# Optimization experiments

Hardware: AMD Instinct MI355X
Metric: run time of the kernel (lower is better)

## Reference

```python
import jax, jax.numpy as jnp
import numpy as np
from jax import lax

D = 1024
K = 3
LN_EPS = 1e-5


def setup_inputs() -> dict:
    key = jax.random.key(0)
    ks = jax.random.split(key, 8)
    B, T = 8, 4096
    x = jax.random.normal(ks[0], (B, T, D), dtype=jnp.float32)
    s = 1.0 / np.sqrt(D)
    in_proj_w = jax.random.uniform(ks[1], (D, 2 * D), jnp.float32, -s, s)
    in_proj_b = jax.random.uniform(ks[2], (2 * D,), jnp.float32, -s, s)
    conv_w = jax.random.uniform(ks[3], (D, 1, K), jnp.float32, -1.0 / np.sqrt(K), 1.0 / np.sqrt(K))
    conv_b = jax.random.uniform(ks[4], (D,), jnp.float32, -1.0 / np.sqrt(K), 1.0 / np.sqrt(K))
    logit_a = jnp.zeros((D,), jnp.float32)
    ssm_b = jnp.full((D,), 0.1, jnp.float32)
    ssm_c = jnp.ones((D,), jnp.float32)
    ssm_d = jnp.zeros((D,), jnp.float32)
    out_proj_w = jax.random.uniform(ks[5], (D, D), jnp.float32, -s, s)
    out_proj_b = jax.random.uniform(ks[6], (D,), jnp.float32, -s, s)
    ln_w = jnp.ones((D,), jnp.float32)
    ln_b = jnp.zeros((D,), jnp.float32)
    return {"x": x, "in_proj_w": in_proj_w, "in_proj_b": in_proj_b,
            "conv_w": conv_w, "conv_b": conv_b, "logit_a": logit_a,
            "ssm_b": ssm_b, "ssm_c": ssm_c, "ssm_d": ssm_d,
            "out_proj_w": out_proj_w, "out_proj_b": out_proj_b,
            "ln_w": ln_w, "ln_b": ln_b}


def _dwconv(v, conv_w, conv_b):
    # v: (B, T, D) -> depthwise conv1d, kernel K, 'same' padding
    vt = jnp.transpose(v, (0, 2, 1))  # (B, D, T)
    out = lax.conv_general_dilated(
        vt, conv_w, window_strides=(1,), padding=[(K // 2, K // 2)],
        dimension_numbers=("NCH", "OIH", "NCH"), feature_group_count=D)
    out = out + conv_b[None, :, None]
    return jnp.transpose(out, (0, 2, 1))  # (B, T, D)


def reference(x, in_proj_w, in_proj_b, conv_w, conv_b, logit_a,
              ssm_b, ssm_c, ssm_d, out_proj_w, out_proj_b, ln_w, ln_b):
    B, T, _ = x.shape
    residual = x
    uv = x @ in_proj_w + in_proj_b                      # (B, T, 2D)
    u, v = uv[..., :D], uv[..., D:]
    v = jax.nn.silu(v)
    v_local = _dwconv(v, conv_w, conv_b)                # (B, T, D)

    a = jax.nn.sigmoid(logit_a).astype(v_local.dtype)
    # diagonal LTI scan: h_t = a*h_{t-1} + b*u_t ; y_t = c*h_t + d*u_t
    def step(h, vt):
        h = a * h + ssm_b * vt
        return h, ssm_c * h + ssm_d * vt
    h0 = jnp.zeros((B, D), v_local.dtype)
    _, y_seq = lax.scan(step, h0, jnp.transpose(v_local, (1, 0, 2)))
    y_seq = jnp.transpose(y_seq, (1, 0, 2))             # (B, T, D)

    out = u * jax.nn.silu(y_seq)
    out = out @ out_proj_w + out_proj_b                 # dropout: eval mode (identity)
    h = out + residual
    mu = jnp.mean(h, axis=-1, keepdims=True)
    var = jnp.mean(jnp.square(h - mu), axis=-1, keepdims=True)
    return (h - mu) * lax.rsqrt(var + LN_EPS) * ln_w + ln_b
```

## Files before the change

kernel.cpp:

```cpp
#include <hip/hip_runtime.h>
#include <cstdint>
#include <cstddef>

#define D_DIM   1024
#define TWO_D   2048
#define B_DIM   8
#define T_DIM   4096
#define BT_DIM  (B_DIM*T_DIM)
#define LN_EPS  1e-5f
#define NCHUNK  128
#define CLEN    (T_DIM/NCHUNK)

typedef __attribute__((ext_vector_type(8))) short bf16x8;
typedef __attribute__((ext_vector_type(4))) float f32x4;

__device__ __forceinline__ float bf2f(unsigned short u){
  union { unsigned int i; float f; } c; c.i = ((unsigned int)u) << 16; return c.f;
}
__device__ __forceinline__ unsigned short f2bf(float f){
  union { float f; unsigned int i; } c; c.f = f;
  unsigned int x = c.i;
  return (unsigned short)((x + 0x7fffu + ((x >> 16) & 1u)) >> 16);
}
__device__ __forceinline__ float sigmoidf_(float x){ return 1.f/(1.f+__expf(-x)); }
__device__ __forceinline__ float siluf_(float x){ return x/(1.f+__expf(-x)); }


__global__ void cvt_f32_bf16(const float* __restrict__ in, unsigned short* __restrict__ out, int n){
  int i = (blockIdx.x*blockDim.x + threadIdx.x)*4;
  const int stride = gridDim.x*blockDim.x*4;
  for (; i + 3 < n; i += stride){
    float4 f = *(const float4*)(in + i);
    ushort4 o; o.x=f2bf(f.x); o.y=f2bf(f.y); o.z=f2bf(f.z); o.w=f2bf(f.w);
    *(ushort4*)(out + i) = o;
  }
}

__global__ __launch_bounds__(256) void cvt_transpose(
    const float* __restrict__ W, unsigned short* __restrict__ Wt,
    int rows, int cols)
{
  __shared__ float tile[32][33];
  const int tx = threadIdx.x & 31;
  const int ty = threadIdx.x >> 5;
  const int tpc = cols >> 5;
  const int bc = blockIdx.x % tpc;
  const int br = blockIdx.x / tpc;
  const int gc = bc*32 + tx;
  const int gr = br*32;
#pragma unroll
  for (int i = 0; i < 32; i += 8)
    tile[ty + i][tx] = W[(size_t)(gr + ty + i)*cols + gc];
  __syncthreads();
#pragma unroll
  for (int i = 0; i < 32; i += 8)
    Wt[(size_t)(bc*32 + ty + i)*rows + gr + tx] = f2bf(tile[tx][ty + i]);
}

template<int EPI>
__global__ __launch_bounds__(512, 2) void gemm256(
    const unsigned short* __restrict__ A,
    const unsigned short* __restrict__ Bt,
    const float* __restrict__ bias,
    const float* __restrict__ resid,
    unsigned short* __restrict__ outU,
    unsigned short* __restrict__ outV,
    float* __restrict__ outF,
    const int K, const int nbn)
{
  __shared__ __align__(16) unsigned short sA[2][2][8192];
  __shared__ __align__(16) unsigned short sB[2][2][8192];

#define BARRIER()   __builtin_amdgcn_s_barrier()
#define FENCE()     __builtin_amdgcn_sched_barrier(0)
#define WAIT_VM4()  do { asm volatile("s_waitcnt vmcnt(4)"); FENCE(); } while(0)
#define WAIT_VM0()  do { asm volatile("s_waitcnt vmcnt(0)"); FENCE(); } while(0)

  const int tid  = threadIdx.x;
  const int lane = tid & 63;
  const int wv   = tid >> 6;
  const int wr   = wv >> 2;
  const int wc   = wv & 3;
  const int fr   = lane & 15;
  const int fq   = lane >> 4;

  const int nwg = gridDim.x;
  const int cpx = nwg >> 3;
  const int wg  = (blockIdx.x & 7) * cpx + (blockIdx.x >> 3);
  const int bm = wg / nbn, bn = wg % nbn;

  const unsigned short* Ag = A  + (size_t)bm * 256 * K;
  const unsigned short* Bg = Bt + (size_t)bn * 256 * K;

  const int r0  = tid >> 2;
  const int r1  = 128 + r0;
  const int c0  = tid & 3;
  const int cs0 = c0 ^ ((r0 >> 1) & 3);
  const int cs1 = c0 ^ ((r1 >> 1) & 3);
  const int ld0 = tid * 8;
  const int ld1 = (512 + tid) * 8;

#define STAGE(ARR, srcp, kofs)                                                           \
  do {                                                                                   \
    __builtin_amdgcn_global_load_lds(                                                    \
      (const __attribute__((address_space(1))) void*)((srcp) + (size_t)r0*K + (kofs) + cs0*8), \
      (__attribute__((address_space(3))) void*)(&(ARR)[ld0]), 16, 0, 0);                 \
    __builtin_amdgcn_global_load_lds(                                                    \
      (const __attribute__((address_space(1))) void*)((srcp) + (size_t)r1*K + (kofs) + cs1*8), \
      (__attribute__((address_space(3))) void*)(&(ARR)[ld1]), 16, 0, 0);                 \
  } while(0)

  const int swz  = fq ^ ((fr >> 1) & 3);
  const int offA = (wr*128 + fr) * 32 + swz * 8;
  const int offB = (wc*64  + fr) * 32 + swz * 8;

  f32x4 acc[8][4];
#pragma unroll
  for (int i = 0; i < 8; ++i)
#pragma unroll
    for (int j = 0; j < 4; ++j) acc[i][j] = {0.f,0.f,0.f,0.f};

  bf16x8 afr[8], bfr[4];

#define PHASE(PAR, KH, STAGE_STMT, TAIL_WAIT)                              \
  do {                                                                     \
    _Pragma("unroll")                                                      \
    for (int m2 = 0; m2 < 8; ++m2)                                         \
      afr[m2] = *(const bf16x8*)(&sA[PAR][KH][offA + m2*512]);             \
    _Pragma("unroll")                                                      \
    for (int n2 = 0; n2 < 4; ++n2)                                         \
      bfr[n2] = *(const bf16x8*)(&sB[PAR][KH][offB + n2*512]);             \
    STAGE_STMT;                                                            \
    BARRIER();                                                             \
    asm volatile("s_waitcnt lgkmcnt(0)");                                  \
    FENCE();                                                               \
    __builtin_amdgcn_s_setprio(1);                                         \
    _Pragma("unroll")                                                      \
    for (int m2 = 0; m2 < 8; ++m2)                                         \
      _Pragma("unroll")                                                    \
      for (int n2 = 0; n2 < 4; ++n2)                                       \
        acc[m2][n2] = __builtin_amdgcn_mfma_f32_16x16x32_bf16(             \
            afr[m2], bfr[n2], acc[m2][n2], 0, 0, 0);                       \
    __builtin_amdgcn_s_setprio(0);                                         \
    TAIL_WAIT;                                                             \
    BARRIER();                                                             \
  } while(0)

  const int npairs = K >> 7;

  STAGE(sA[0][0], Ag, 0);
  STAGE(sB[0][0], Bg, 0);
  STAGE(sA[0][1], Ag, 32);
  STAGE(sB[0][1], Bg, 32);
  WAIT_VM4();
  BARRIER();

  for (int i = 0; i < npairs - 1; ++i){
    const int kbO = ((i << 1) + 1) << 6;
    const int kbE = ((i << 1) + 2) << 6;
    PHASE(0, 0, { STAGE(sA[1][0], Ag, kbO);      STAGE(sB[1][0], Bg, kbO);      }, WAIT_VM4());
    PHASE(0, 1, { STAGE(sA[1][1], Ag, kbO + 32); STAGE(sB[1][1], Bg, kbO + 32); }, WAIT_VM4());
    PHASE(1, 0, { STAGE(sA[0][0], Ag, kbE);      STAGE(sB[0][0], Bg, kbE);      }, WAIT_VM4());
    PHASE(1, 1, { STAGE(sA[0][1], Ag, kbE + 32); STAGE(sB[0][1], Bg, kbE + 32); }, WAIT_VM4());
  }
  PHASE(0, 0, { STAGE(sA[1][0], Ag, K - 64); STAGE(sB[1][0], Bg, K - 64); }, WAIT_VM4());
  PHASE(0, 1, { STAGE(sA[1][1], Ag, K - 32); STAGE(sB[1][1], Bg, K - 32); }, WAIT_VM4());
  PHASE(1, 0, , WAIT_VM0());
  PHASE(1, 1, , );

  const int nb = bn*256 + wc*64;
  const int mb = bm*256 + wr*128;
  float bsv[4];
#pragma unroll
  for (int ni = 0; ni < 4; ++ni) bsv[ni] = bias[nb + ni*16 + fr];

  if (EPI == 0){
    const bool isV = (nb >= D_DIM);
    unsigned short* dst = isV ? (outV + (nb - D_DIM)) : (outU + nb);
#pragma unroll
    for (int mi = 0; mi < 8; ++mi){
#pragma unroll
      for (int j = 0; j < 4; ++j){
        const int m = mb + mi*16 + fq*4 + j;
        unsigned short* row = dst + (size_t)m*D_DIM + fr;
#pragma unroll
        for (int ni = 0; ni < 4; ++ni){
          float cv = acc[mi][ni][j] + bsv[ni];
          row[ni*16] = f2bf(isV ? siluf_(cv) : cv);
        }
      }
    }
  } else {
#pragma unroll
    for (int mi = 0; mi < 8; ++mi){
#pragma unroll
      for (int j = 0; j < 4; ++j){
        const int m = mb + mi*16 + fq*4 + j;
        const float* rrow = resid + (size_t)m*D_DIM + nb + fr;
        float* orow = outF + (size_t)m*D_DIM + nb + fr;
#pragma unroll
        for (int ni = 0; ni < 4; ++ni)
          orow[ni*16] = acc[mi][ni][j] + bsv[ni] + rrow[ni*16];
      }
    }
  }
#undef PHASE
#undef STAGE
#undef BARRIER
#undef FENCE
#undef WAIT_VM4
#undef WAIT_VM0
}

__global__ __launch_bounds__(256) void scan_a(
    const unsigned short* __restrict__ v,
    const float* __restrict__ conv_w, const float* __restrict__ conv_b,
    const float* __restrict__ logit_a, const float* __restrict__ ssm_b,
    float* __restrict__ hend)
{
  const int b = blockIdx.x / NCHUNK;
  const int c = blockIdx.x % NCHUNK;
  const int d0 = threadIdx.x * 4;
  const int t0 = c * CLEN;
  const unsigned short* vb = v + (size_t)b * T_DIM * D_DIM;

  float w0[4], w1[4], w2[4], av[4], bv[4], cb[4];
#pragma unroll
  for (int i=0;i<4;i++){
    w0[i] = conv_w[(d0+i)*3+0];
    w1[i] = conv_w[(d0+i)*3+1];
    w2[i] = conv_w[(d0+i)*3+2];
    cb[i] = conv_b[d0+i];
    av[i] = sigmoidf_(logit_a[d0+i]);
    bv[i] = ssm_b[d0+i];
  }
  float vm1[4], v0[4], h[4] = {0.f,0.f,0.f,0.f};
  if (t0 == 0){
#pragma unroll
    for (int i=0;i<4;i++) vm1[i]=0.f;
  } else {
    ushort4 u = *(const ushort4*)(vb + (size_t)(t0-1)*D_DIM + d0);
    vm1[0]=bf2f(u.x); vm1[1]=bf2f(u.y); vm1[2]=bf2f(u.z); vm1[3]=bf2f(u.w);
  }
  {
    ushort4 u = *(const ushort4*)(vb + (size_t)t0*D_DIM + d0);
    v0[0]=bf2f(u.x); v0[1]=bf2f(u.y); v0[2]=bf2f(u.z); v0[3]=bf2f(u.w);
  }
#pragma unroll 8
  for (int t = t0; t < t0 + CLEN; ++t){
    float vp1[4];
    if (t + 1 < T_DIM){
      ushort4 u = *(const ushort4*)(vb + (size_t)(t+1)*D_DIM + d0);
      vp1[0]=bf2f(u.x); vp1[1]=bf2f(u.y); vp1[2]=bf2f(u.z); vp1[3]=bf2f(u.w);
    } else { vp1[0]=vp1[1]=vp1[2]=vp1[3]=0.f; }
#pragma unroll
    for (int i=0;i<4;i++){
      float vl = w0[i]*vm1[i] + w1[i]*v0[i] + w2[i]*vp1[i] + cb[i];
      h[i] = av[i]*h[i] + bv[i]*vl;
      vm1[i]=v0[i]; v0[i]=vp1[i];
    }
  }
  float* he = hend + ((size_t)b*NCHUNK + c)*D_DIM + d0;
#pragma unroll
  for (int i=0;i<4;i++) he[i] = h[i];
}

__global__ void scan_fix(const float* __restrict__ hend, const float* __restrict__ logit_a,
                         float* __restrict__ hinit)
{
  int idx = blockIdx.x*blockDim.x + threadIdx.x;
  if (idx >= B_DIM*D_DIM) return;
  const int b = idx / D_DIM, d = idx % D_DIM;
  const float a  = sigmoidf_(logit_a[d]);
  const float aL = __powf(a, (float)CLEN);
  float h = 0.f;
  for (int c = 0; c < NCHUNK; ++c){
    hinit[((size_t)b*NCHUNK + c)*D_DIM + d] = h;
    h = aL*h + hend[((size_t)b*NCHUNK + c)*D_DIM + d];
  }
}

__global__ __launch_bounds__(256) void scan_c(
    const unsigned short* __restrict__ v,
    const unsigned short* __restrict__ ubuf,
    const float* __restrict__ conv_w, const float* __restrict__ conv_b,
    const float* __restrict__ logit_a, const float* __restrict__ ssm_b,
    const float* __restrict__ ssm_c, const float* __restrict__ ssm_d,
    const float* __restrict__ hinit,
    unsigned short* __restrict__ gated)
{
  const int b = blockIdx.x / NCHUNK;
  const int c = blockIdx.x % NCHUNK;
  const int d0 = threadIdx.x * 4;
  const int t0 = c * CLEN;
  const unsigned short* vb = v    + (size_t)b * T_DIM * D_DIM;
  const unsigned short* ub = ubuf + (size_t)b * T_DIM * D_DIM;
  unsigned short* gb       = gated+ (size_t)b * T_DIM * D_DIM;

  float w0[4], w1[4], w2[4], av[4], bv[4], cb[4], scv[4], sdv[4], h[4];
#pragma unroll
  for (int i=0;i<4;i++){
    w0[i] = conv_w[(d0+i)*3+0];
    w1[i] = conv_w[(d0+i)*3+1];
    w2[i] = conv_w[(d0+i)*3+2];
    cb[i] = conv_b[d0+i];
    av[i] = sigmoidf_(logit_a[d0+i]);
    bv[i] = ssm_b[d0+i];
    scv[i] = ssm_c[d0+i];
    sdv[i] = ssm_d[d0+i];
    h[i] = hinit[((size_t)b*NCHUNK + c)*D_DIM + d0 + i];
  }
  float vm1[4], v0[4];
  if (t0 == 0){
#pragma unroll
    for (int i=0;i<4;i++) vm1[i]=0.f;
  } else {
    ushort4 u = *(const ushort4*)(vb + (size_t)(t0-1)*D_DIM + d0);
    vm1[0]=bf2f(u.x); vm1[1]=bf2f(u.y); vm1[2]=bf2f(u.z); vm1[3]=bf2f(u.w);
  }
  {
    ushort4 u = *(const ushort4*)(vb + (size_t)t0*D_DIM + d0);
    v0[0]=bf2f(u.x); v0[1]=bf2f(u.y); v0[2]=bf2f(u.z); v0[3]=bf2f(u.w);
  }
#pragma unroll 8
  for (int t = t0; t < t0 + CLEN; ++t){
    float vp1[4];
    if (t + 1 < T_DIM){
      ushort4 u = *(const ushort4*)(vb + (size_t)(t+1)*D_DIM + d0);
      vp1[0]=bf2f(u.x); vp1[1]=bf2f(u.y); vp1[2]=bf2f(u.z); vp1[3]=bf2f(u.w);
    } else { vp1[0]=vp1[1]=vp1[2]=vp1[3]=0.f; }
    ushort4 uu = *(const ushort4*)(ub + (size_t)t*D_DIM + d0);
    float uf[4] = { bf2f(uu.x), bf2f(uu.y), bf2f(uu.z), bf2f(uu.w) };
    ushort4 go;
    unsigned short gtmp[4];
#pragma unroll
    for (int i=0;i<4;i++){
      float vl = w0[i]*vm1[i] + w1[i]*v0[i] + w2[i]*vp1[i] + cb[i];
      h[i] = av[i]*h[i] + bv[i]*vl;
      float y = scv[i]*h[i] + sdv[i]*vl;
      gtmp[i] = f2bf(uf[i] * siluf_(y));
      vm1[i]=v0[i]; v0[i]=vp1[i];
    }
    go.x=gtmp[0]; go.y=gtmp[1]; go.z=gtmp[2]; go.w=gtmp[3];
    *(ushort4*)(gb + (size_t)t*D_DIM + d0) = go;
  }
}

__global__ __launch_bounds__(256) void ln_kernel(
    float* __restrict__ io, const float* __restrict__ lw, const float* __restrict__ lb)
{
  __shared__ float rs[4], rq[4];
  const int row = blockIdx.x;
  const int tid = threadIdx.x;
  float* p = io + (size_t)row * D_DIM;
  float4 x = *(const float4*)(p + tid*4);
  float s = x.x + x.y + x.z + x.w;
  float q = x.x*x.x + x.y*x.y + x.z*x.z + x.w*x.w;
#pragma unroll
  for (int off = 32; off > 0; off >>= 1){
    s += __shfl_down(s, off, 64);
    q += __shfl_down(q, off, 64);
  }
  const int wv = tid >> 6;
  if ((tid & 63) == 0){ rs[wv] = s; rq[wv] = q; }
  __syncthreads();
  const float ts = rs[0]+rs[1]+rs[2]+rs[3];
  const float tq = rq[0]+rq[1]+rq[2]+rq[3];
  const float mu  = ts * (1.f/(float)D_DIM);
  const float var = tq * (1.f/(float)D_DIM) - mu*mu;
  const float inv = rsqrtf(var + LN_EPS);
  const float4 w4 = *(const float4*)(lw + tid*4);
  const float4 b4 = *(const float4*)(lb + tid*4);
  float4 o;
  o.x = (x.x-mu)*inv*w4.x + b4.x;
  o.y = (x.y-mu)*inv*w4.y + b4.y;
  o.z = (x.z-mu)*inv*w4.z + b4.z;
  o.w = (x.w-mu)*inv*w4.w + b4.w;
  *(float4*)(p + tid*4) = o;
}

extern "C" void kernel_launch(void* const* d_in, const int* in_sizes, int n_in,
                              void* d_out, int out_size, void* d_ws, size_t ws_size,
                              hipStream_t stream)
{
  const float* x     = (const float*)d_in[0];
  const float* w1    = (const float*)d_in[1];
  const float* b1    = (const float*)d_in[2];
  const float* convw = (const float*)d_in[3];
  const float* convb = (const float*)d_in[4];
  const float* la    = (const float*)d_in[5];
  const float* sb    = (const float*)d_in[6];
  const float* sc    = (const float*)d_in[7];
  const float* sd    = (const float*)d_in[8];
  const float* w2    = (const float*)d_in[9];
  const float* b2    = (const float*)d_in[10];
  const float* lw    = (const float*)d_in[11];
  const float* lb    = (const float*)d_in[12];
  float* out = (float*)d_out;

  char* ws = (char*)d_ws;
  unsigned short* xb    = (unsigned short*)(ws + 0);
  unsigned short* ubf   = (unsigned short*)(ws + 67108864);
  unsigned short* vbf   = (unsigned short*)(ws + 134217728);
  unsigned short* w1t   = (unsigned short*)(ws + 201326592);
  unsigned short* w2t   = (unsigned short*)(ws + 205520896);
  float*          hend  = (float*)(ws + 207618048);
  float*          hinit = (float*)(ws + 211812352);

  cvt_f32_bf16<<<2048, 256, 0, stream>>>(x, xb, BT_DIM*D_DIM);
  cvt_transpose<<<(D_DIM/32)*(TWO_D/32), 256, 0, stream>>>(w1, w1t, D_DIM, TWO_D);
  cvt_transpose<<<(D_DIM/32)*(D_DIM/32), 256, 0, stream>>>(w2, w2t, D_DIM, D_DIM);

  gemm256<0><<<dim3((BT_DIM/256)*(TWO_D/256)), 512, 0, stream>>>(
      xb, w1t, b1, nullptr, ubf, vbf, nullptr, D_DIM, TWO_D/256);

  scan_a<<<B_DIM*NCHUNK, 256, 0, stream>>>(vbf, convw, convb, la, sb, hend);
  scan_fix<<<(B_DIM*D_DIM + 255)/256, 256, 0, stream>>>(hend, la, hinit);
  scan_c<<<B_DIM*NCHUNK, 256, 0, stream>>>(vbf, ubf, convw, convb, la, sb, sc, sd, hinit, xb);

  gemm256<1><<<dim3((BT_DIM/256)*(D_DIM/256)), 512, 0, stream>>>(
      xb, w2t, b2, x, nullptr, nullptr, out, D_DIM, D_DIM/256);

  ln_kernel<<<BT_DIM, 256, 0, stream>>>(out, lw, lb);
}
```

Baseline: 426.9 us.

## Replace pipelined 256x256 GEMM with simple single-buffered 128x128 GEMM

The GEMM kernel moves from a 256x256 tile with 512 threads, double-buffered LDS and hand-scheduled phases (setprio, explicit waitcnt) to a 128x128 tile with 256 threads and a plain single-buffered load/sync/compute loop. The aim is higher occupancy and more workgroups. The cost is losing the overlap of global loads with MFMA and halving data reuse per tile, which raises global and LDS traffic. scan_fix also batches its 8 strided hend loads ahead of the serial recurrence to expose memory parallelism.

```diff
diff --git a/kernel.cpp b/kernel.cpp
--- a/kernel.cpp
+++ b/kernel.cpp
@@ -58,7 +58,7 @@
 }
 
 template<int EPI>
-__global__ __launch_bounds__(512, 2) void gemm256(
+__global__ __launch_bounds__(256, 4) void gemm128(
     const unsigned short* __restrict__ A,
     const unsigned short* __restrict__ Bt,
     const float* __restrict__ bias,
@@ -68,19 +68,14 @@
     float* __restrict__ outF,
     const int K, const int nbn)
 {
-  __shared__ __align__(16) unsigned short sA[2][2][8192];
-  __shared__ __align__(16) unsigned short sB[2][2][8192];
-
-#define BARRIER()   __builtin_amdgcn_s_barrier()
-#define FENCE()     __builtin_amdgcn_sched_barrier(0)
-#define WAIT_VM4()  do { asm volatile("s_waitcnt vmcnt(4)"); FENCE(); } while(0)
-#define WAIT_VM0()  do { asm volatile("s_waitcnt vmcnt(0)"); FENCE(); } while(0)
+  __shared__ __align__(16) unsigned short As[128*32];
+  __shared__ __align__(16) unsigned short Bs[128*32];
 
   const int tid  = threadIdx.x;
   const int lane = tid & 63;
   const int wv   = tid >> 6;
-  const int wr   = wv >> 2;
-  const int wc   = wv & 3;
+  const int wr   = wv >> 1;
+  const int wc   = wv & 1;
   const int fr   = lane & 15;
   const int fq   = lane >> 4;
 
@@ -89,16 +84,16 @@
   const int wg  = (blockIdx.x & 7) * cpx + (blockIdx.x >> 3);
   const int bm = wg / nbn, bn = wg % nbn;
 
-  const unsigned short* Ag = A  + (size_t)bm * 256 * K;
-  const unsigned short* Bg = Bt + (size_t)bn * 256 * K;
+  const unsigned short* Ag = A  + (size_t)bm * 128 * K;
+  const unsigned short* Bg = Bt + (size_t)bn * 128 * K;
 
   const int r0  = tid >> 2;
-  const int r1  = 128 + r0;
+  const int r1  = 64 + r0;
   const int c0  = tid & 3;
   const int cs0 = c0 ^ ((r0 >> 1) & 3);
   const int cs1 = c0 ^ ((r1 >> 1) & 3);
   const int ld0 = tid * 8;
-  const int ld1 = (512 + tid) * 8;
+  const int ld1 = (256 + tid) * 8;
 
 #define STAGE(ARR, srcp, kofs)                                                           \
   do {                                                                                   \
@@ -111,65 +106,36 @@
   } while(0)
 
   const int swz  = fq ^ ((fr >> 1) & 3);
-  const int offA = (wr*128 + fr) * 32 + swz * 8;
-  const int offB = (wc*64  + fr) * 32 + swz * 8;
-
-  f32x4 acc[8][4];
-#pragma unroll
-  for (int i = 0; i < 8; ++i)
+  const int offA = (wr*64 + fr) * 32 + swz * 8;
+  const int offB = (wc*64 + fr) * 32 + swz * 8;
+
+  f32x4 acc[4][4];
+#pragma unroll
+  for (int i = 0; i < 4; ++i)
 #pragma unroll
     for (int j = 0; j < 4; ++j) acc[i][j] = {0.f,0.f,0.f,0.f};
 
-  bf16x8 afr[8], bfr[4];
-
-#define PHASE(PAR, KH, STAGE_STMT, TAIL_WAIT)                              \
-  do {                                                                     \
-    _Pragma("unroll")                                                      \
-    for (int m2 = 0; m2 < 8; ++m2)                                         \
-      afr[m2] = *(const bf16x8*)(&sA[PAR][KH][offA + m2*512]);             \
-    _Pragma("unroll")                                                      \
-    for (int n2 = 0; n2 < 4; ++n2)                                         \
-      bfr[n2] = *(const bf16x8*)(&sB[PAR][KH][offB + n2*512]);             \
-    STAGE_STMT;                                                            \
-    BARRIER();                                                             \
-    asm volatile("s_waitcnt lgkmcnt(0)");                                  \
-    FENCE();                                                               \
-    __builtin_amdgcn_s_setprio(1);                                         \
-    _Pragma("unroll")                                                      \
-    for (int m2 = 0; m2 < 8; ++m2)                                         \
-      _Pragma("unroll")                                                    \
-      for (int n2 = 0; n2 < 4; ++n2)                                       \
-        acc[m2][n2] = __builtin_amdgcn_mfma_f32_16x16x32_bf16(             \
-            afr[m2], bfr[n2], acc[m2][n2], 0, 0, 0);                       \
-    __builtin_amdgcn_s_setprio(0);                                         \
-    TAIL_WAIT;                                                             \
-    BARRIER();                                                             \
-  } while(0)
-
-  const int npairs = K >> 7;
-
-  STAGE(sA[0][0], Ag, 0);
-  STAGE(sB[0][0], Bg, 0);
-  STAGE(sA[0][1], Ag, 32);
-  STAGE(sB[0][1], Bg, 32);
-  WAIT_VM4();
-  BARRIER();
-
-  for (int i = 0; i < npairs - 1; ++i){
-    const int kbO = ((i << 1) + 1) << 6;
-    const int kbE = ((i << 1) + 2) << 6;
-    PHASE(0, 0, { STAGE(sA[1][0], Ag, kbO);      STAGE(sB[1][0], Bg, kbO);      }, WAIT_VM4());
-    PHASE(0, 1, { STAGE(sA[1][1], Ag, kbO + 32); STAGE(sB[1][1], Bg, kbO + 32); }, WAIT_VM4());
-    PHASE(1, 0, { STAGE(sA[0][0], Ag, kbE);      STAGE(sB[0][0], Bg, kbE);      }, WAIT_VM4());
-    PHASE(1, 1, { STAGE(sA[0][1], Ag, kbE + 32); STAGE(sB[0][1], Bg, kbE + 32); }, WAIT_VM4());
-  }
-  PHASE(0, 0, { STAGE(sA[1][0], Ag, K - 64); STAGE(sB[1][0], Bg, K - 64); }, WAIT_VM4());
-  PHASE(0, 1, { STAGE(sA[1][1], Ag, K - 32); STAGE(sB[1][1], Bg, K - 32); }, WAIT_VM4());
-  PHASE(1, 0, , WAIT_VM0());
-  PHASE(1, 1, , );
-
-  const int nb = bn*256 + wc*64;
-  const int mb = bm*256 + wr*128;
+  for (int kt = 0; kt < K; kt += 32){
+    STAGE(As, Ag, kt);
+    STAGE(Bs, Bg, kt);
+    __syncthreads();
+
+    bf16x8 af[4], bf[4];
+#pragma unroll
+    for (int mi = 0; mi < 4; ++mi) af[mi] = *(const bf16x8*)(&As[offA + mi*512]);
+#pragma unroll
+    for (int ni = 0; ni < 4; ++ni) bf[ni] = *(const bf16x8*)(&Bs[offB + ni*512]);
+#pragma unroll
+    for (int mi = 0; mi < 4; ++mi)
+#pragma unroll
+      for (int ni = 0; ni < 4; ++ni)
+        acc[mi][ni] = __builtin_amdgcn_mfma_f32_16x16x32_bf16(af[mi], bf[ni], acc[mi][ni], 0, 0, 0);
+    __syncthreads();
+  }
+#undef STAGE
+
+  const int nb = bn*128 + wc*64;
+  const int mb = bm*128 + wr*64;
   float bsv[4];
 #pragma unroll
   for (int ni = 0; ni < 4; ++ni) bsv[ni] = bias[nb + ni*16 + fr];
@@ -178,7 +144,7 @@
     const bool isV = (nb >= D_DIM);
     unsigned short* dst = isV ? (outV + (nb - D_DIM)) : (outU + nb);
 #pragma unroll
-    for (int mi = 0; mi < 8; ++mi){
+    for (int mi = 0; mi < 4; ++mi){
 #pragma unroll
       for (int j = 0; j < 4; ++j){
         const int m = mb + mi*16 + fq*4 + j;
@@ -192,7 +158,7 @@
     }
   } else {
 #pragma unroll
-    for (int mi = 0; mi < 8; ++mi){
+    for (int mi = 0; mi < 4; ++mi){
 #pragma unroll
       for (int j = 0; j < 4; ++j){
         const int m = mb + mi*16 + fq*4 + j;
@@ -204,12 +170,6 @@
       }
     }
   }
-#undef PHASE
-#undef STAGE
-#undef BARRIER
-#undef FENCE
-#undef WAIT_VM4
-#undef WAIT_VM0
 }
 
 __global__ __launch_bounds__(256) void scan_a(
@@ -273,10 +233,19 @@
   const int b = idx / D_DIM, d = idx % D_DIM;
   const float a  = sigmoidf_(logit_a[d]);
   const float aL = __powf(a, (float)CLEN);
+  const float* hep = hend  + (size_t)b*NCHUNK*D_DIM + d;
+  float*       hip = hinit + (size_t)b*NCHUNK*D_DIM + d;
   float h = 0.f;
-  for (int c = 0; c < NCHUNK; ++c){
-    hinit[((size_t)b*NCHUNK + c)*D_DIM + d] = h;
-    h = aL*h + hend[((size_t)b*NCHUNK + c)*D_DIM + d];
+  for (int cb = 0; cb < NCHUNK; cb += 8){
+    float buf[8];
+#pragma unroll
+    for (int j = 0; j < 8; ++j)
+      buf[j] = hep[(size_t)(cb + j)*D_DIM];
+#pragma unroll
+    for (int j = 0; j < 8; ++j){
+      hip[(size_t)(cb + j)*D_DIM] = h;
+      h = aL*h + buf[j];
+    }
   }
 }
 
@@ -411,15 +380,15 @@
   cvt_transpose<<<(D_DIM/32)*(TWO_D/32), 256, 0, stream>>>(w1, w1t, D_DIM, TWO_D);
   cvt_transpose<<<(D_DIM/32)*(D_DIM/32), 256, 0, stream>>>(w2, w2t, D_DIM, D_DIM);
 
-  gemm256<0><<<dim3((BT_DIM/256)*(TWO_D/256)), 512, 0, stream>>>(
-      xb, w1t, b1, nullptr, ubf, vbf, nullptr, D_DIM, TWO_D/256);
+  gemm128<0><<<dim3((BT_DIM/128)*(TWO_D/128)), 256, 0, stream>>>(
+      xb, w1t, b1, nullptr, ubf, vbf, nullptr, D_DIM, TWO_D/128);
 
   scan_a<<<B_DIM*NCHUNK, 256, 0, stream>>>(vbf, convw, convb, la, sb, hend);
   scan_fix<<<(B_DIM*D_DIM + 255)/256, 256, 0, stream>>>(hend, la, hinit);
   scan_c<<<B_DIM*NCHUNK, 256, 0, stream>>>(vbf, ubf, convw, convb, la, sb, sc, sd, hinit, xb);
 
-  gemm256<1><<<dim3((BT_DIM/256)*(D_DIM/256)), 512, 0, stream>>>(
-      xb, w2t, b2, x, nullptr, nullptr, out, D_DIM, D_DIM/256);
+  gemm128<1><<<dim3((BT_DIM/128)*(D_DIM/128)), 256, 0, stream>>>(
+      xb, w2t, b2, x, nullptr, nullptr, out, D_DIM, D_DIM/128);
 
   ln_kernel<<<BT_DIM, 256, 0, stream>>>(out, lw, lb);
 }
```

New measurement: 434.9 us. No clear change (+1.9%).
